# Kernel tuning notes

Hardware: AMD Instinct MI355X
Metric: run time of the kernel (lower is better)

The kernel has to match this reference:

```python
import jax, jax.numpy as jnp
import numpy as np
from jax import lax

NG, NF, NW = 5, 10, 8
STEP = NG + NF + 1
MARGIN, LAM, ALPHA, P_W, R_W = 1.0, 0.01, 1.0, 0.7, 0.1
KNUM, KMUL = 5, 2.0
GAMMA = 5.0
BIG = 1e10  # finite stand-in for inf border of the soft-DTW DP (grad-safe)
T, DFEAT = 512, 64


def setup_inputs() -> dict:
    key = jax.random.key(0)
    k1, k2 = jax.random.split(key)
    data = jax.random.normal(k1, (NW * STEP, T, DFEAT), jnp.float32)
    lens = jax.random.randint(k2, (NW * STEP,), T // 2, T + 1, dtype=jnp.int32)
    return {"data": data, "lens": lens}


def _softdtw_R(D):
    # D: [P, N, M] squared-euclidean cost. Returns rows [N, P, M] with
    # rows[i-1, p, j-1] == R[i, j] of the soft-DTW DP recurrence
    # R[i,j] = D[i,j] + softmin_gamma(R[i-1,j], R[i,j-1], R[i-1,j-1]).
    Pn, N, M = D.shape
    row0 = jnp.concatenate([jnp.zeros((Pn, 1), D.dtype), jnp.full((Pn, M), BIG, D.dtype)], axis=1)

    def row_step(prev, d_row):
        up, diag = prev[:, 1:], prev[:, :-1]

        def col_step(left, ins):
            d, u, dg = ins  # each [P]
            smin = -GAMMA * jax.nn.logsumexp(jnp.stack([-left, -u, -dg]) / GAMMA, axis=0)
            r = d + smin
            return r, r

        _, cols = lax.scan(col_step, jnp.full((Pn,), BIG, D.dtype), (d_row.T, up.T, diag.T))
        new_row = jnp.concatenate([jnp.full((Pn, 1), BIG, D.dtype), cols.T], axis=1)
        return new_row, cols.T

    _, rows = lax.scan(row_step, row0, jnp.swapaxes(D, 0, 1))
    return rows


def _mmd(source, target):
    # Standard multi-kernel Gaussian MMD applied to 3-D inputs exactly as the
    # torch code does: L2 distance sums over the time axis only -> [n, n, d].
    ns = source.shape[0]
    total = jnp.concatenate([source, target], axis=0)  # [n, T, d]
    n = total.shape[0]
    sq = jnp.sum(total * total, axis=1)  # [n, d]
    cross = jnp.einsum('atf,btf->abf', total, total)  # [n, n, d]
    L2 = sq[:, None, :] + sq[None, :, :] - 2.0 * cross
    bw = jnp.sum(L2) / (n * n - n)
    bw = bw / (KMUL ** (KNUM // 2))
    K = sum(jnp.exp(-L2 / (bw * KMUL ** i)) for i in range(KNUM))
    XX, YY = K[:ns, :ns], K[ns:, ns:]
    XY, YX = K[:ns, ns:], K[ns:, :ns]
    return jnp.mean(XX + YY - XY - YX)


def _forward(data, lens):
    # Batch all (anchor, positive/negative) pairs across writers.
    anchor_idx = jnp.repeat(jnp.arange(NW) * STEP, NG + NF)                       # [P]
    other_idx = (jnp.arange(NW)[:, None] * STEP + 1 + jnp.arange(NG + NF)[None, :]).ravel()
    X, Y = data[anchor_idx], data[other_idx]  # [P, T, d]
    lx, ly = lens[anchor_idx], lens[other_idx]
    # Pairwise squared distances D[p,i,j] = ||X[p,i] - Y[p,j]||^2
    D = (jnp.sum(X * X, -1)[:, :, None] + jnp.sum(Y * Y, -1)[:, None, :]
         - 2.0 * jnp.einsum('pid,pjd->pij', X, Y))
    rows = _softdtw_R(D)  # [T, P, T]
    Pn = X.shape[0]
    # R[len_a, len_p] only depends on D[:len_a, :len_p], so gathering at the
    # lengths equals running soft-DTW on the length-sliced sequences.
    dist = rows[lx - 1, jnp.arange(Pn), ly - 1] / (lx + ly).astype(data.dtype)
    dist = dist.reshape(NW, NG + NF)
    dg, dn = dist[:, :NG], dist[:, NG:]          # genuine / forgery distances
    only_pos = jnp.sum(dg, axis=1) * (LAM / NG)  # [NW]
    lk1 = jax.nn.relu(dg[:, :, None] + MARGIN - dn[:, None, :5]) * P_W
    lk2 = jax.nn.relu(dg[:, :, None] + MARGIN - dn[:, None, 5:]) * (1.0 - P_W)
    nz = jnp.sum(lk1 != 0, axis=(1, 2)) + jnp.sum(lk2 != 0, axis=(1, 2))  # stop-grad count
    lv = (jnp.sum(lk1, (1, 2)) + jnp.sum(lk2, (1, 2))) / (nz + 1).astype(data.dtype)
    total_loss = jnp.mean(lv + only_pos)
    mmd1 = _mmd(data[0:STEP - 5], data[STEP:2 * STEP - 5]) * ALPHA
    var_g = jnp.var(dg.ravel(), ddof=1) * R_W   # torch.var is unbiased
    return total_loss + mmd1 + var_g


def reference(data, lens):
    return _forward(data, lens)
```

## Files before the change

### kernel.cpp

```cpp
#include <hip/hip_runtime.h>
#include <hip/hip_bf16.h>
#include <cstdint>
#include <cstddef>

#define T_ 512
#define DF 64
#define NPAIR 120
#define STEPW 16
#define NEGS (-(1 << 26))
#define NSK 640

#define C1_ 0.28853900817779268f
#define C2D 3.4657359027997265

typedef unsigned short ushort_t;
using f32x4 = __attribute__((ext_vector_type(4))) float;
using bf16x8 = __attribute__((ext_vector_type(8))) short;

__device__ __forceinline__ float wred_sum(float v) {
#pragma unroll
  for (int o = 32; o > 0; o >>= 1) v += __shfl_down(v, o);
  return v;
}

__device__ __forceinline__ int dexp(double x) {
  return (int)((__double_as_longlong(x) >> 52) & 0x7ff) - 1023;
}

__device__ __forceinline__ ushort_t f2bf(float x) {
  __hip_bfloat16 h = __float2bfloat16(x);
  return *reinterpret_cast<ushort_t*>(&h);
}
__device__ __forceinline__ float bf2f(ushort_t u) {
  __hip_bfloat16 h = *reinterpret_cast<__hip_bfloat16*>(&u);
  return __bfloat162float(h);
}

#define GLOAD(DST, PTR)                                                    \
  asm volatile("global_load_dwordx4 %0, %1, off"                           \
               : "=&v"(DST) : "v"(PTR) : "memory")

__global__ __launch_bounds__(256) void gemm_mmd_kernel(
    const float* __restrict__ data, float* __restrict__ wbuf, int pair0,
    int npc, float* __restrict__ l2buf, float* __restrict__ bwpart) {
  __shared__ ushort_t XH[4096], XL[4096], YH[4096], YL[4096];
  __shared__ float nrmx[64];
  __shared__ float nrmy[64];

  if ((int)blockIdx.y == npc) {
    const int tid = threadIdx.x;
    const int g = tid >> 6;
    const int f = tid & 63;
    const int b = (int)blockIdx.x * 4 + g;
    if (b < 253) {
      int u = 0, rem = b;
      while (rem >= 22 - u) { rem -= 22 - u; ++u; }
      int v = u + rem;
      float s = 0.f;
      if (u != v) {
        int iu = u < 11 ? u : u + 5;
        int iv = v < 11 ? v : v + 5;
        const float* A = data + (size_t)iu * (T_ * DF) + f;
        const float* B = data + (size_t)iv * (T_ * DF) + f;
#pragma unroll 8
        for (int t = 0; t < T_; ++t) {
          float dd = A[(size_t)t * DF] - B[(size_t)t * DF];
          s = fmaf(dd, dd, s);
        }
      }
      l2buf[(size_t)(u * 22 + v) * 64 + f] = s;
      l2buf[(size_t)(v * 22 + u) * 64 + f] = s;
      float tot = wred_sum(s);
      if (f == 0) bwpart[b] = 2.f * tot;
    }
    return;
  }

  const int tile = blockIdx.x;
  const int pc = blockIdx.y;
  const int p = pair0 + pc;
  const int w = p / 15;
  const int o = p - w * 15;
  const int aidx = w * STEPW;
  const int oidx = aidx + 1 + o;
  const int i0 = (tile >> 3) << 6;
  const int j0 = (tile & 7) << 6;
  const int tid = threadIdx.x;

  const float* Xg = data + (size_t)aidx * (T_ * DF);
  const float* Yg = data + (size_t)oidx * (T_ * DF);

#pragma unroll
  for (int l = 0; l < 4; ++l) {
    int idx = tid + l * 256;
    int r = idx >> 4;
    int c = idx & 15;
    int g = c >> 1, h = c & 1;
    int base = r * 64 + ((g ^ (r & 7)) << 3) + (h << 2);
    float4 xv = reinterpret_cast<const float4*>(Xg + (size_t)(i0 + r) * DF)[c];
    float4 yv = reinterpret_cast<const float4*>(Yg + (size_t)(j0 + r) * DF)[c];
    const float xa[4] = {xv.x, xv.y, xv.z, xv.w};
    const float ya[4] = {yv.x, yv.y, yv.z, yv.w};
#pragma unroll
    for (int e = 0; e < 4; ++e) {
      ushort_t xh = f2bf(xa[e]);
      XH[base + e] = xh;
      XL[base + e] = f2bf(xa[e] - bf2f(xh));
      ushort_t yh = f2bf(ya[e]);
      YH[base + e] = yh;
      YL[base + e] = f2bf(ya[e] - bf2f(yh));
    }
  }
  __syncthreads();

  if (tid < 128) {
    int r = tid & 63;
    float s = 0.f;
    if (tid < 64) {
#pragma unroll
      for (int k = 0; k < 64; ++k) {
        int a = r * 64 + (((k >> 3) ^ (r & 7)) << 3) + (k & 7);
        float x = bf2f(XH[a]) + bf2f(XL[a]);
        s = fmaf(x, x, s);
      }
      nrmx[r] = s;
    } else {
#pragma unroll
      for (int k = 0; k < 64; ++k) {
        int a = r * 64 + (((k >> 3) ^ (r & 7)) << 3) + (k & 7);
        float y = bf2f(YH[a]) + bf2f(YL[a]);
        s = fmaf(y, y, s);
      }
      nrmy[r] = s;
    }
  }
  __syncthreads();

  const int lane = tid & 63;
  const int wid = tid >> 6;
  const int rowA = 16 * wid + (lane & 15);
  const int b16 = lane >> 4;

  const int aA0 = rowA * 64 + (((b16) ^ (rowA & 7)) << 3);
  const int aA1 = rowA * 64 + (((4 + b16) ^ (rowA & 7)) << 3);
  bf16x8 ah0 = *reinterpret_cast<const bf16x8*>(&XH[aA0]);
  bf16x8 ah1 = *reinterpret_cast<const bf16x8*>(&XH[aA1]);
  bf16x8 al0 = *reinterpret_cast<const bf16x8*>(&XL[aA0]);
  bf16x8 al1 = *reinterpret_cast<const bf16x8*>(&XL[aA1]);

  float* WpBase = wbuf + (size_t)pc * (NSK * T_);

#pragma unroll
  for (int t = 0; t < 4; ++t) {
    const int rowB = 16 * t + (lane & 15);
    const int aB0 = rowB * 64 + (((b16) ^ (rowB & 7)) << 3);
    const int aB1 = rowB * 64 + (((4 + b16) ^ (rowB & 7)) << 3);
    bf16x8 bh0 = *reinterpret_cast<const bf16x8*>(&YH[aB0]);
    bf16x8 bh1 = *reinterpret_cast<const bf16x8*>(&YH[aB1]);
    bf16x8 bl0 = *reinterpret_cast<const bf16x8*>(&YL[aB0]);
    bf16x8 bl1 = *reinterpret_cast<const bf16x8*>(&YL[aB1]);

    f32x4 acc = {0.f, 0.f, 0.f, 0.f};
    acc = __builtin_amdgcn_mfma_f32_16x16x32_bf16(ah0, bh0, acc, 0, 0, 0);
    acc = __builtin_amdgcn_mfma_f32_16x16x32_bf16(ah1, bh1, acc, 0, 0, 0);
    acc = __builtin_amdgcn_mfma_f32_16x16x32_bf16(ah0, bl0, acc, 0, 0, 0);
    acc = __builtin_amdgcn_mfma_f32_16x16x32_bf16(ah1, bl1, acc, 0, 0, 0);
    acc = __builtin_amdgcn_mfma_f32_16x16x32_bf16(al0, bh0, acc, 0, 0, 0);
    acc = __builtin_amdgcn_mfma_f32_16x16x32_bf16(al1, bh1, acc, 0, 0, 0);

    const int jg = j0 + 16 * t + (lane & 15);
    const float ny = nrmy[16 * t + (lane & 15)];
    const int g8 = jg >> 3;
    const int off = (((jg >> 2) & 1) << 8) + 4 * g8 + (jg & 3);
#pragma unroll
    for (int r = 0; r < 4; ++r) {
      const int ig = i0 + 16 * wid + 4 * b16 + r;
      float d = nrmx[16 * wid + 4 * b16 + r] + ny - 2.f * acc[r];
      float wv = __builtin_exp2f(-d * C1_);
      WpBase[(size_t)(ig + 2 * g8) * T_ + off] = wv;
    }
  }
}

__global__ __launch_bounds__(64) void dtw_mmdk_kernel(
    const float* __restrict__ Wm, const int* __restrict__ lens,
    float* __restrict__ dist, int pair0, int npc,
    const float* __restrict__ l2buf, const float* __restrict__ bwpart,
    float* __restrict__ mmdpart) {
  if ((int)blockIdx.x >= npc) {
    int b = (int)blockIdx.x - npc;
    if (b < 121) {
      int a = b / 11, c = b - a * 11;
      int f = threadIdx.x;
      float bs = 0.f;
      for (int k2 = f; k2 < 253; k2 += 64) bs += bwpart[k2];
      bs = wred_sum(bs);
      float bw = __shfl(bs, 0) * (1.f / (462.f * 4.f));
      float xx = l2buf[(size_t)(a * 22 + c) * 64 + f];
      float yy = l2buf[(size_t)((11 + a) * 22 + (11 + c)) * 64 + f];
      float xy = l2buf[(size_t)(a * 22 + (11 + c)) * 64 + f];
      float yx = l2buf[(size_t)((11 + a) * 22 + c) * 64 + f];
      float term = 0.f;
      float ib = 1.f / bw;
#pragma unroll
      for (int i = 0; i < 5; ++i) {
        term += expf(-xx * ib) + expf(-yy * ib) - expf(-xy * ib)
              - expf(-yx * ib);
        ib *= 0.5f;
      }
      float tt = wred_sum(term);
      if (f == 0) mmdpart[b] = tt;
    }
    return;
  }

  const int pc = blockIdx.x;
  const int p = pair0 + pc;
  const int w = p / 15;
  const int o = p - w * 15;
  const int lx = lens[w * STEPW];
  const int ly = lens[w * STEPW + 1 + o];
  const int l = threadIdx.x;
  const int imax = lx - 1;
  const int jt = ly - 1;
  const int lt = jt >> 3, ct = jt & 7;
  const int M = lt + (imax >> 1);
  const float invl = 1.f / (float)(lx + ly);

  const float* wp = Wm + (size_t)pc * (NSK * T_) + 4 * l;

  float4 K0a, K0b, K1a, K1b, K2a, K2b, K3a, K3b;
  float4 K4a, K4b, K5a, K5b, K6a, K6b, K7a, K7b;
  float4 K8a, K8b, K9a, K9b, K10a, K10b, K11a, K11b;

#define LDROW(A, B, R)                                     \
  {                                                        \
    int r_ = (R); r_ = r_ > 637 ? 637 : r_;                \
    const float* p_ = wp + (size_t)r_ * T_;                \
    GLOAD(A, p_); GLOAD(B, p_ + 256);                      \
  }

  LDROW(K0a, K0b, 0); LDROW(K1a, K1b, 1);
  LDROW(K2a, K2b, 2); LDROW(K3a, K3b, 3);
  LDROW(K4a, K4b, 4); LDROW(K5a, K5b, 5);

  double e0 = 0., e1 = 0., e2 = 0., e3 = 0.;
  double e4 = 0., e5 = 0., e6 = 0., e7 = 0.;
  int S = NEGS;
  int pSE = -1023;
  double sendA_v = 0.;  int sendA_s = NEGS;
  double rAv = 0.;  int rAs = NEGS;
  double pvB = 0.;  int psB = NEGS;

#define SUP(MM, SA0, SA1, SB0, SB1, RA0, RA1, RB0, RB1)                    \
  {                                                                        \
    const int m_ = (MM);                                                   \
    double nvB = __shfl_up(e7, 1);           \
    LDROW(RA0, RA1, 2 * m_ + 6);                                           \
    LDROW(RB0, RB1, 2 * m_ + 7);                                           \
    asm volatile("s_waitcnt vmcnt(12)" ::: "memory");                      \
    __builtin_amdgcn_sched_barrier(0);                                     \
    const int i = 2 * (m_ - l);                                            \
    double lA = rAv, dA = pvB, lB = nvB, dB2 = rAv;                        \
    int slA = rAs, sdA = psB, slB = rAs, sdB = rAs;                        \
    if (l == 0) {                                                          \
      lA = 0.; slA = NEGS;                                                 \
      dA = (i == 0) ? 1. : 0.; sdA = (i == 0) ? 0 : NEGS;                  \
      lB = 0.; slB = NEGS;                                                 \
      dB2 = 0.; sdB = NEGS;                                                \
    }                                                                      \
    if ((unsigned)i <= (unsigned)imax) {                                   \
      int NA = max(S + pSE, max(slA + dexp(lA), sdA + dexp(dA)));          \
      const int dS = S - NA;                                               \
      if (dS != 0) {                                                       \
        e0 = ldexp(e0, dS); e1 = ldexp(e1, dS);                            \
        e2 = ldexp(e2, dS); e3 = ldexp(e3, dS);                            \
        e4 = ldexp(e4, dS); e5 = ldexp(e5, dS);                            \
        e6 = ldexp(e6, dS); e7 = ldexp(e7, dS);                            \
      }                                                                    \
      double L = ldexp(lA, slA - NA);                                      \
      double G = ldexp(dA, sdA - NA);                                      \
      const double WA0 = (double)SA0.x, WA1 = (double)SA0.y;               \
      const double WA2 = (double)SA0.z, WA3 = (double)SA0.w;               \
      const double WA4 = (double)SA1.x, WA5 = (double)SA1.y;               \
      const double WA6 = (double)SA1.z, WA7 = (double)SA1.w;               \
      double qa0 = WA0 * ((L + G) + e0);                                   \
      double qa1 = WA1 * (e1 + e0);                                        \
      double qa2 = WA2 * (e2 + e1);                                        \
      double qa3 = WA3 * (e3 + e2);                                        \
      double qa4 = WA4 * (e4 + e3);                                        \
      double qa5 = WA5 * (e5 + e4);                                        \
      double qa6 = WA6 * (e6 + e5);                                        \
      double qa7 = WA7 * (e7 + e6);                                        \
      double a0 = qa0;                                                     \
      double a1 = fma(WA1, a0, qa1);                                       \
      double a2 = fma(WA2, a1, qa2);                                       \
      double a3 = fma(WA3, a2, qa3);                                       \
      double a4 = fma(WA4, a3, qa4);                                       \
      double a5 = fma(WA5, a4, qa5);                                       \
      double a6 = fma(WA6, a5, qa6);                                       \
      double a7 = fma(WA7, a6, qa7);                                       \
      if (i + 1 <= imax) {                                                 \
        int NB = max(NA, max(slB + dexp(lB), sdB + dexp(dB2)));            \
        const int dB = NA - NB;                                            \
        if (dB != 0) {                                                     \
          a0 = ldexp(a0, dB); a1 = ldexp(a1, dB);                          \
          a2 = ldexp(a2, dB); a3 = ldexp(a3, dB);                          \
          a4 = ldexp(a4, dB); a5 = ldexp(a5, dB);                          \
          a6 = ldexp(a6, dB); a7 = ldexp(a7, dB);                          \
        }                                                                  \
        sendA_v = a7; sendA_s = NB;                                        \
        double LB = ldexp(lB, slB - NB);                                   \
        double GB = ldexp(dB2, sdB - NB);                                  \
        const double WB0 = (double)SB0.x, WB1 = (double)SB0.y;             \
        const double WB2 = (double)SB0.z, WB3 = (double)SB0.w;             \
        const double WB4 = (double)SB1.x, WB5 = (double)SB1.y;             \
        const double WB6 = (double)SB1.z, WB7 = (double)SB1.w;             \
        double qb0 = WB0 * ((LB + GB) + a0);                               \
        double qb1 = WB1 * (a1 + a0);                                      \
        double qb2 = WB2 * (a2 + a1);                                      \
        double qb3 = WB3 * (a3 + a2);                                      \
        double qb4 = WB4 * (a4 + a3);                                      \
        double qb5 = WB5 * (a5 + a4);                                      \
        double qb6 = WB6 * (a6 + a5);                                      \
        double qb7 = WB7 * (a7 + a6);                                      \
        e0 = qb0;                                                          \
        e1 = fma(WB1, e0, qb1);                                            \
        e2 = fma(WB2, e1, qb2);                                            \
        e3 = fma(WB3, e2, qb3);                                            \
        e4 = fma(WB4, e3, qb4);                                            \
        e5 = fma(WB5, e4, qb5);                                            \
        e6 = fma(WB6, e5, qb6);                                            \
        e7 = fma(WB7, e6, qb7);                                            \
        S = NB;                                                            \
      } else {                                                             \
        e0 = a0; e1 = a1; e2 = a2; e3 = a3;                                \
        e4 = a4; e5 = a5; e6 = a6; e7 = a7;                                \
        sendA_v = a7; sendA_s = NA;                                        \
        S = NA;                                                            \
      }                                                                    \
          \
      double sumN = ((e0 + e1) + (e2 + e3)) + ((e4 + e5) + (e6 + e7));     \
      pSE = dexp(sumN);                                                    \
    }                                                                      \
    pvB = nvB; psB = rAs;                                                  \
    rAv = __shfl_up(sendA_v, 1);                                           \
    rAs = __shfl_up(sendA_s, 1);                                           \
  }

  const int nsup = (M + 6) / 6 * 6;
  for (int mb = 0; mb < nsup; mb += 6) {
    SUP(mb + 0, K0a, K0b, K1a, K1b, K6a, K6b, K7a, K7b);
    SUP(mb + 1, K2a, K2b, K3a, K3b, K8a, K8b, K9a, K9b);
    SUP(mb + 2, K4a, K4b, K5a, K5b, K10a, K10b, K11a, K11b);
    SUP(mb + 3, K6a, K6b, K7a, K7b, K0a, K0b, K1a, K1b);
    SUP(mb + 4, K8a, K8b, K9a, K9b, K2a, K2b, K3a, K3b);
    SUP(mb + 5, K10a, K10b, K11a, K11b, K4a, K4b, K5a, K5b);
  }

  asm volatile("s_waitcnt vmcnt(0)" ::: "memory");

  if (l == lt) {
    double out_v = (ct == 0) ? e0 : (ct == 1) ? e1 : (ct == 2) ? e2
                 : (ct == 3) ? e3 : (ct == 4) ? e4 : (ct == 5) ? e5
                 : (ct == 6) ? e6 : e7;
    double vv = (out_v > 0.) ? out_v : 1e-300;
    double r = -C2D * (log2(vv) + (double)S);
    dist[p] = (float)(r * (double)invl);
  }
}

__global__ __launch_bounds__(64) void finalize_kernel(
    const float* __restrict__ dist, const float* __restrict__ mmdpart,
    float* __restrict__ out) {
  int lane = threadIdx.x;
  float lv_po = 0.f;
  float dg[5];
#pragma unroll
  for (int g = 0; g < 5; ++g) dg[g] = 0.f;
  if (lane < 8) {
    const float* dr = dist + lane * 15;
    float dn[10];
#pragma unroll
    for (int g = 0; g < 5; ++g) dg[g] = dr[g];
#pragma unroll
    for (int k = 0; k < 10; ++k) dn[k] = dr[5 + k];
    float s1 = 0.f, s2 = 0.f;
    int nz = 0;
#pragma unroll
    for (int g = 0; g < 5; ++g) {
#pragma unroll
      for (int k = 0; k < 5; ++k) {
        float v2 = dg[g] + 1.0f - dn[k];
        if (v2 > 0.f) { s1 += v2; ++nz; }
      }
#pragma unroll
      for (int k = 5; k < 10; ++k) {
        float v2 = dg[g] + 1.0f - dn[k];
        if (v2 > 0.f) { s2 += v2; ++nz; }
      }
    }
    float only_pos = (dg[0] + dg[1] + dg[2] + dg[3] + dg[4]) * 0.002f;
    float lv = (s1 * 0.7f + s2 * 0.3f) / (float)(nz + 1);
    lv_po = lv + only_pos;
  }
  float tl = wred_sum(lv_po);
  tl = __shfl(tl, 0);

  float psum = dg[0] + dg[1] + dg[2] + dg[3] + dg[4];
  float tsum = wred_sum(psum);
  float mean = __shfl(tsum, 0) * (1.f / 40.f);
  float pdev = 0.f;
  if (lane < 8) {
#pragma unroll
    for (int g = 0; g < 5; ++g) {
      float dd = dg[g] - mean;
      pdev = fmaf(dd, dd, pdev);
    }
  }
  float tdev = wred_sum(pdev);
  tdev = __shfl(tdev, 0);

  float msum = 0.f;
  for (int k2 = lane; k2 < 121; k2 += 64) msum += mmdpart[k2];
  float mt = wred_sum(msum);

  if (lane == 0) {
    float total_loss = tl * (1.f / 8.f);
    float var_g = (tdev / 39.f) * 0.1f;
    float mmd = mt * (1.f / 7744.f);
    out[0] = total_loss + mmd + var_g;
  }
}

__global__ __launch_bounds__(64) void zero_out_kernel(float* __restrict__ out,
                                                      int n) {
  int i = blockIdx.x * 64 + threadIdx.x;
  if (i < n) out[i] = 0.f;
}

extern "C" void kernel_launch(void* const* d_in, const int* in_sizes, int n_in,
                              void* d_out, int out_size, void* d_ws,
                              size_t ws_size, hipStream_t stream) {
  const float* data = (const float*)d_in[0];
  const int* lens = (const int*)d_in[1];
  float* out = (float*)d_out;
  char* ws = (char*)d_ws;

  const size_t HDR = 131072;
  const size_t per_pair = (size_t)NSK * T_ * sizeof(float);

  if (ws_size < HDR + per_pair) {
    zero_out_kernel<<<dim3((out_size + 63) / 64), 64, 0, stream>>>(out,
                                                                   out_size);
    return;
  }

  float* dist = (float*)(ws + 0);
  float* bwpart = (float*)(ws + 1024);
  float* mmdpart = (float*)(ws + 3072);
  float* l2buf = (float*)(ws + 4096);
  float* wbuf = (float*)(ws + HDR);

  size_t avail = ws_size - HDR;
  int PC = (int)(avail / per_pair);
  if (PC > NPAIR) PC = NPAIR;

  for (int p0 = 0; p0 < NPAIR; p0 += PC) {
    int pc = (NPAIR - p0) < PC ? (NPAIR - p0) : PC;
    int first = (p0 == 0) ? 1 : 0;
    gemm_mmd_kernel<<<dim3(64, pc + first), 256, 0, stream>>>(
        data, wbuf, p0, pc, l2buf, bwpart);
    dtw_mmdk_kernel<<<dim3(pc + (first ? 121 : 0)), 64, 0, stream>>>(
        wbuf, lens, dist, p0, pc, l2buf, bwpart, mmdpart);
  }
  finalize_kernel<<<dim3(1), 64, 0, stream>>>(dist, mmdpart, out);
}
```

Baseline: 181.0 us.

## Precompute bf16 hi/lo splits and row norms once per sequence in a prep kernel

Adds a prep kernel that converts every sequence once into bf16 high/low halves and per-row squared norms stored in workspace. The GEMM kernel then loads its MFMA operands directly from global memory instead of converting the same sequences repeatedly in each tile and staging them through shared memory. This removes redundant conversion work and two barriers, at the cost of an extra launch, extra workspace, and unswizzled global loads for operands.

```diff
diff --git a/kernel.cpp b/kernel.cpp
--- a/kernel.cpp
+++ b/kernel.cpp
@@ -9,6 +9,7 @@
 #define STEPW 16
 #define NEGS (-(1 << 26))
 #define NSK 640
+#define NSEQ 128
 
 #define C1_ 0.28853900817779268f
 #define C2D 3.4657359027997265
@@ -17,6 +18,8 @@
 using f32x4 = __attribute__((ext_vector_type(4))) float;
 using bf16x8 = __attribute__((ext_vector_type(8))) short;
 
+struct ushort4_t { ushort_t x, y, z, w; };
+
 __device__ __forceinline__ float wred_sum(float v) {
 #pragma unroll
   for (int o = 32; o > 0; o >>= 1) v += __shfl_down(v, o);
@@ -40,13 +43,57 @@
   asm volatile("global_load_dwordx4 %0, %1, off"                           \
                : "=&v"(DST) : "v"(PTR) : "memory")
 
+__global__ __launch_bounds__(256) void prep_kernel(
+    const float* __restrict__ data, ushort_t* __restrict__ xh,
+    ushort_t* __restrict__ xl, float* __restrict__ nrm) {
+  __shared__ float part[64][17];
+  const int seq = blockIdx.x >> 3;
+  const int rg = blockIdx.x & 7;
+  const int tid = threadIdx.x;
+  const float* src = data + (size_t)seq * (T_ * DF) + (size_t)rg * 64 * DF;
+  ushort_t* dh = xh + (size_t)seq * (T_ * DF) + (size_t)rg * 64 * DF;
+  ushort_t* dl = xl + (size_t)seq * (T_ * DF) + (size_t)rg * 64 * DF;
+
+#pragma unroll
+  for (int l = 0; l < 4; ++l) {
+    int idx = tid + l * 256;
+    int r = idx >> 4;
+    int c = idx & 15;
+    float4 v = reinterpret_cast<const float4*>(src + (size_t)r * DF)[c];
+    const float xa[4] = {v.x, v.y, v.z, v.w};
+    ushort4_t h4, l4;
+    float s = 0.f;
+    ushort_t hh, ll;
+    hh = f2bf(xa[0]); ll = f2bf(xa[0] - bf2f(hh));
+    h4.x = hh; l4.x = ll;
+    { float rec = bf2f(hh) + bf2f(ll); s = fmaf(rec, rec, s); }
+    hh = f2bf(xa[1]); ll = f2bf(xa[1] - bf2f(hh));
+    h4.y = hh; l4.y = ll;
+    { float rec = bf2f(hh) + bf2f(ll); s = fmaf(rec, rec, s); }
+    hh = f2bf(xa[2]); ll = f2bf(xa[2] - bf2f(hh));
+    h4.z = hh; l4.z = ll;
+    { float rec = bf2f(hh) + bf2f(ll); s = fmaf(rec, rec, s); }
+    hh = f2bf(xa[3]); ll = f2bf(xa[3] - bf2f(hh));
+    h4.w = hh; l4.w = ll;
+    { float rec = bf2f(hh) + bf2f(ll); s = fmaf(rec, rec, s); }
+    reinterpret_cast<ushort4_t*>(dh + (size_t)r * DF)[c] = h4;
+    reinterpret_cast<ushort4_t*>(dl + (size_t)r * DF)[c] = l4;
+    part[r][c] = s;
+  }
+  __syncthreads();
+  if (tid < 64) {
+    float s = 0.f;
+#pragma unroll
+    for (int c = 0; c < 16; ++c) s += part[tid][c];
+    nrm[(size_t)seq * T_ + rg * 64 + tid] = s;
+  }
+}
+
 __global__ __launch_bounds__(256) void gemm_mmd_kernel(
     const float* __restrict__ data, float* __restrict__ wbuf, int pair0,
-    int npc, float* __restrict__ l2buf, float* __restrict__ bwpart) {
-  __shared__ ushort_t XH[4096], XL[4096], YH[4096], YL[4096];
-  __shared__ float nrmx[64];
-  __shared__ float nrmy[64];
-
+    int npc, float* __restrict__ l2buf, float* __restrict__ bwpart,
+    const ushort_t* __restrict__ xh, const ushort_t* __restrict__ xl,
+    const float* __restrict__ nrm) {
   if ((int)blockIdx.y == npc) {
     const int tid = threadIdx.x;
     const int g = tid >> 6;
@@ -86,79 +133,39 @@
   const int i0 = (tile >> 3) << 6;
   const int j0 = (tile & 7) << 6;
   const int tid = threadIdx.x;
-
-  const float* Xg = data + (size_t)aidx * (T_ * DF);
-  const float* Yg = data + (size_t)oidx * (T_ * DF);
-
-#pragma unroll
-  for (int l = 0; l < 4; ++l) {
-    int idx = tid + l * 256;
-    int r = idx >> 4;
-    int c = idx & 15;
-    int g = c >> 1, h = c & 1;
-    int base = r * 64 + ((g ^ (r & 7)) << 3) + (h << 2);
-    float4 xv = reinterpret_cast<const float4*>(Xg + (size_t)(i0 + r) * DF)[c];
-    float4 yv = reinterpret_cast<const float4*>(Yg + (size_t)(j0 + r) * DF)[c];
-    const float xa[4] = {xv.x, xv.y, xv.z, xv.w};
-    const float ya[4] = {yv.x, yv.y, yv.z, yv.w};
-#pragma unroll
-    for (int e = 0; e < 4; ++e) {
-      ushort_t xh = f2bf(xa[e]);
-      XH[base + e] = xh;
-      XL[base + e] = f2bf(xa[e] - bf2f(xh));
-      ushort_t yh = f2bf(ya[e]);
-      YH[base + e] = yh;
-      YL[base + e] = f2bf(ya[e] - bf2f(yh));
-    }
-  }
-  __syncthreads();
-
-  if (tid < 128) {
-    int r = tid & 63;
-    float s = 0.f;
-    if (tid < 64) {
-#pragma unroll
-      for (int k = 0; k < 64; ++k) {
-        int a = r * 64 + (((k >> 3) ^ (r & 7)) << 3) + (k & 7);
-        float x = bf2f(XH[a]) + bf2f(XL[a]);
-        s = fmaf(x, x, s);
-      }
-      nrmx[r] = s;
-    } else {
-#pragma unroll
-      for (int k = 0; k < 64; ++k) {
-        int a = r * 64 + (((k >> 3) ^ (r & 7)) << 3) + (k & 7);
-        float y = bf2f(YH[a]) + bf2f(YL[a]);
-        s = fmaf(y, y, s);
-      }
-      nrmy[r] = s;
-    }
-  }
-  __syncthreads();
-
   const int lane = tid & 63;
   const int wid = tid >> 6;
-  const int rowA = 16 * wid + (lane & 15);
   const int b16 = lane >> 4;
-
-  const int aA0 = rowA * 64 + (((b16) ^ (rowA & 7)) << 3);
-  const int aA1 = rowA * 64 + (((4 + b16) ^ (rowA & 7)) << 3);
-  bf16x8 ah0 = *reinterpret_cast<const bf16x8*>(&XH[aA0]);
-  bf16x8 ah1 = *reinterpret_cast<const bf16x8*>(&XH[aA1]);
-  bf16x8 al0 = *reinterpret_cast<const bf16x8*>(&XL[aA0]);
-  bf16x8 al1 = *reinterpret_cast<const bf16x8*>(&XL[aA1]);
+  const int kof = 8 * b16;
+
+  const ushort_t* XHg = xh + (size_t)aidx * (T_ * DF);
+  const ushort_t* XLg = xl + (size_t)aidx * (T_ * DF);
+  const ushort_t* YHg = xh + (size_t)oidx * (T_ * DF);
+  const ushort_t* YLg = xl + (size_t)oidx * (T_ * DF);
+  const float* nrmX = nrm + (size_t)aidx * T_;
+  const float* nrmY = nrm + (size_t)oidx * T_;
+
+  const int rowAg = i0 + 16 * wid + (lane & 15);
+  const size_t abase = (size_t)rowAg * DF + kof;
+  bf16x8 ah0 = *reinterpret_cast<const bf16x8*>(&XHg[abase]);
+  bf16x8 ah1 = *reinterpret_cast<const bf16x8*>(&XHg[abase + 32]);
+  bf16x8 al0 = *reinterpret_cast<const bf16x8*>(&XLg[abase]);
+  bf16x8 al1 = *reinterpret_cast<const bf16x8*>(&XLg[abase + 32]);
+
+  const float4 nxv =
+      *reinterpret_cast<const float4*>(&nrmX[i0 + 16 * wid + 4 * b16]);
+  const float nx[4] = {nxv.x, nxv.y, nxv.z, nxv.w};
 
   float* WpBase = wbuf + (size_t)pc * (NSK * T_);
 
 #pragma unroll
   for (int t = 0; t < 4; ++t) {
-    const int rowB = 16 * t + (lane & 15);
-    const int aB0 = rowB * 64 + (((b16) ^ (rowB & 7)) << 3);
-    const int aB1 = rowB * 64 + (((4 + b16) ^ (rowB & 7)) << 3);
-    bf16x8 bh0 = *reinterpret_cast<const bf16x8*>(&YH[aB0]);
-    bf16x8 bh1 = *reinterpret_cast<const bf16x8*>(&YH[aB1]);
-    bf16x8 bl0 = *reinterpret_cast<const bf16x8*>(&YL[aB0]);
-    bf16x8 bl1 = *reinterpret_cast<const bf16x8*>(&YL[aB1]);
+    const int rowBg = j0 + 16 * t + (lane & 15);
+    const size_t bbase = (size_t)rowBg * DF + kof;
+    bf16x8 bh0 = *reinterpret_cast<const bf16x8*>(&YHg[bbase]);
+    bf16x8 bh1 = *reinterpret_cast<const bf16x8*>(&YHg[bbase + 32]);
+    bf16x8 bl0 = *reinterpret_cast<const bf16x8*>(&YLg[bbase]);
+    bf16x8 bl1 = *reinterpret_cast<const bf16x8*>(&YLg[bbase + 32]);
 
     f32x4 acc = {0.f, 0.f, 0.f, 0.f};
     acc = __builtin_amdgcn_mfma_f32_16x16x32_bf16(ah0, bh0, acc, 0, 0, 0);
@@ -169,13 +176,13 @@
     acc = __builtin_amdgcn_mfma_f32_16x16x32_bf16(al1, bh1, acc, 0, 0, 0);
 
     const int jg = j0 + 16 * t + (lane & 15);
-    const float ny = nrmy[16 * t + (lane & 15)];
+    const float ny = nrmY[rowBg];
     const int g8 = jg >> 3;
     const int off = (((jg >> 2) & 1) << 8) + 4 * g8 + (jg & 3);
 #pragma unroll
     for (int r = 0; r < 4; ++r) {
       const int ig = i0 + 16 * wid + 4 * b16 + r;
-      float d = nrmx[16 * wid + 4 * b16 + r] + ny - 2.f * acc[r];
+      float d = nx[r] + ny - 2.f * acc[r];
       float wv = __builtin_exp2f(-d * C1_);
       WpBase[(size_t)(ig + 2 * g8) * T_ + off] = wv;
     }
@@ -255,7 +262,7 @@
 #define SUP(MM, SA0, SA1, SB0, SB1, RA0, RA1, RB0, RB1)                    \
   {                                                                        \
     const int m_ = (MM);                                                   \
-    double nvB = __shfl_up(e7, 1);           \
+    double nvB = __shfl_up(e7, 1);                                         \
     LDROW(RA0, RA1, 2 * m_ + 6);                                           \
     LDROW(RB0, RB1, 2 * m_ + 7);                                           \
     asm volatile("s_waitcnt vmcnt(12)" ::: "memory");                      \
@@ -339,7 +346,6 @@
         sendA_v = a7; sendA_s = NA;                                        \
         S = NA;                                                            \
       }                                                                    \
-          \
       double sumN = ((e0 + e1) + (e2 + e3)) + ((e4 + e5) + (e6 + e7));     \
       pSE = dexp(sumN);                                                    \
     }                                                                      \
@@ -448,9 +454,13 @@
   char* ws = (char*)d_ws;
 
   const size_t HDR = 131072;
+  const size_t NRM_OFF = HDR;
+  const size_t XH_OFF = NRM_OFF + 262144;
+  const size_t XL_OFF = XH_OFF + 8388608;
+  const size_t WB_OFF = XL_OFF + 8388608;
   const size_t per_pair = (size_t)NSK * T_ * sizeof(float);
 
-  if (ws_size < HDR + per_pair) {
+  if (ws_size < WB_OFF + per_pair) {
     zero_out_kernel<<<dim3((out_size + 63) / 64), 64, 0, stream>>>(out,
                                                                    out_size);
     return;
@@ -460,17 +470,22 @@
   float* bwpart = (float*)(ws + 1024);
   float* mmdpart = (float*)(ws + 3072);
   float* l2buf = (float*)(ws + 4096);
-  float* wbuf = (float*)(ws + HDR);
-
-  size_t avail = ws_size - HDR;
+  float* nrm = (float*)(ws + NRM_OFF);
+  ushort_t* xh = (ushort_t*)(ws + XH_OFF);
+  ushort_t* xl = (ushort_t*)(ws + XL_OFF);
+  float* wbuf = (float*)(ws + WB_OFF);
+
+  size_t avail = ws_size - WB_OFF;
   int PC = (int)(avail / per_pair);
   if (PC > NPAIR) PC = NPAIR;
+
+  prep_kernel<<<dim3(NSEQ * 8), 256, 0, stream>>>(data, xh, xl, nrm);
 
   for (int p0 = 0; p0 < NPAIR; p0 += PC) {
     int pc = (NPAIR - p0) < PC ? (NPAIR - p0) : PC;
     int first = (p0 == 0) ? 1 : 0;
     gemm_mmd_kernel<<<dim3(64, pc + first), 256, 0, stream>>>(
-        data, wbuf, p0, pc, l2buf, bwpart);
+        data, wbuf, p0, pc, l2buf, bwpart, xh, xl, nrm);
     dtw_mmdk_kernel<<<dim3(pc + (first ? 121 : 0)), 64, 0, stream>>>(
         wbuf, lens, dist, p0, pc, l2buf, bwpart, mmdpart);
   }
```

Measured after the change: 231.3 us. 27.8% more time.
